# Optimization experiments

Hardware: AMD Instinct MI355X
Metric: run time of the kernel (lower is better)

## Reference

```python
import jax, jax.numpy as jnp
import numpy as np

N_NODES = 100000
N_EDGES = 1600000
D = 64
EPS_NORM = 1e-9
EPS_DENOM = 1e-9


def setup_inputs() -> dict:
    key = jax.random.key(0)
    k1, k2, k3, k4, k5 = jax.random.split(key, 5)
    x = jax.random.normal(k1, (N_NODES, D), dtype=jnp.float32)
    z = jax.random.normal(k2, (N_NODES, D), dtype=jnp.float32)
    edge_index = jax.random.randint(k3, (2, N_EDGES), 0, N_NODES, dtype=jnp.int64)
    W = jax.random.normal(k4, (D, D), dtype=jnp.float32) * (1.0 / np.sqrt(D))
    b = jax.random.normal(k5, (D,), dtype=jnp.float32) * 0.01
    alpha = jnp.ones((), dtype=jnp.float32)
    bias_edge = jnp.zeros((), dtype=jnp.float32)
    return {"x": x, "edge_index": edge_index, "z": z, "W": W, "b": b,
            "alpha": alpha, "bias_edge": bias_edge}


def reference(x, edge_index, z, W, b, alpha, bias_edge):
    row, col = edge_index[0], edge_index[1]
    z_i = z[row]                      # [E, D] gather
    z_j = z[col]                      # [E, D] gather
    num = jnp.sum(z_i * z_j, axis=-1)                       # [E]
    den = jnp.maximum(jnp.linalg.norm(z_i, axis=-1) * jnp.linalg.norm(z_j, axis=-1), EPS_NORM)
    corr = num / den                                        # cosine correlation per edge
    logits = alpha * corr + bias_edge                       # [E]
    exp_logits = jnp.exp(logits - jnp.max(logits))          # global-max-stabilized exp
    denom = jax.ops.segment_sum(exp_logits, row, num_segments=N_NODES)  # [N]
    attn = exp_logits / (denom[row] + EPS_DENOM)            # edge softmax over incoming edges
    msgs = attn[:, None] * x[col]                           # [E, D]
    out = jax.ops.segment_sum(msgs, row, num_segments=N_NODES)          # [N, D]
    return out @ W.T + b                                    # Linear(in_dim, out_dim)
```

## Files before the change

### kernel.cpp

```cpp
#include <hip/hip_runtime.h>
#include <hip/hip_fp16.h>
#include <math.h>

#define NN 100000
#define NE 1600000
#define D  64
#define NBLK 391

typedef _Float16 half2v __attribute__((ext_vector_type(2)));

__device__ __forceinline__ unsigned int pack_entry(int col, float ex) {
    unsigned short hb = __half_as_ushort(__float2half(ex));
    return ((unsigned int)col << 15) | (unsigned int)(hb & 0x7FFFu);
}
__device__ __forceinline__ float unpack_ex(unsigned int pk) {
    return __half2float(__ushort_as_half((unsigned short)(pk & 0x7FFFu)));
}

__global__ __launch_bounds__(256) void k_prep_count(const float* __restrict__ z,
                                                    const float* __restrict__ x,
                                                    const float* __restrict__ W,
                                                    __half* __restrict__ zx,
                                                    const int* __restrict__ ei,
                                                    int* __restrict__ cnt,
                                                    unsigned int* __restrict__ rankr) {
    __shared__ float Wt[64 * 65];
    for (int i = threadIdx.x; i < 4096; i += 256) {
        Wt[(i & 63) * 65 + (i >> 6)] = W[i];
    }
    __syncthreads();
    const int lane = threadIdx.x & 63;
    int wave = blockIdx.x * 4 + (threadIdx.x >> 6);
    int nWaves = gridDim.x * 4;
    for (int n = wave; n < NN; n += nWaves) {
        float zv = z[n * D + lane];
        float s = zv * zv;
#pragma unroll
        for (int off = 32; off; off >>= 1) s += __shfl_xor(s, off);
        float inv = 1.0f / sqrtf(fmaxf(s, 1e-18f));
        zx[(size_t)n * 128 + lane] = __float2half(zv * inv);
        float xv = x[n * D + lane];
        float y0 = 0.0f, y1 = 0.0f, y2 = 0.0f, y3 = 0.0f;
#pragma unroll
        for (int d = 0; d < 64; d += 4) {
            y0 = fmaf(__shfl(xv, d), Wt[d * 65 + lane], y0);
            y1 = fmaf(__shfl(xv, d + 1), Wt[(d + 1) * 65 + lane], y1);
            y2 = fmaf(__shfl(xv, d + 2), Wt[(d + 2) * 65 + lane], y2);
            y3 = fmaf(__shfl(xv, d + 3), Wt[(d + 3) * 65 + lane], y3);
        }
        zx[(size_t)n * 128 + 64 + lane] = __float2half((y0 + y1) + (y2 + y3));
    }
    int i = blockIdx.x * 256 + threadIdx.x;
    int stride = gridDim.x * 256;
    for (int e = i; e < NE; e += stride) {
        int r = __builtin_nontemporal_load(&ei[e]);
        int rk = atomicAdd(&cnt[r], 1);
        __builtin_nontemporal_store(((unsigned int)r << 15) | (unsigned int)rk, &rankr[e]);
    }
}

__global__ __launch_bounds__(256) void k_scan1(const int* __restrict__ cnt,
                                               int* __restrict__ inc,
                                               int* __restrict__ bsum) {
    __shared__ int sh[256];
    int gid = blockIdx.x * 256 + threadIdx.x;
    int v = (gid < NN) ? cnt[gid] : 0;
    sh[threadIdx.x] = v;
    __syncthreads();
    for (int off = 1; off < 256; off <<= 1) {
        int t = (threadIdx.x >= off) ? sh[threadIdx.x - off] : 0;
        __syncthreads();
        sh[threadIdx.x] += t;
        __syncthreads();
    }
    if (gid < NN) inc[gid] = sh[threadIdx.x];
    if (threadIdx.x == 255) bsum[blockIdx.x] = sh[255];
}

__global__ __launch_bounds__(512) void k_scan2(int* __restrict__ bsum) {
    __shared__ int sh[512];
    int v = (threadIdx.x < NBLK) ? bsum[threadIdx.x] : 0;
    sh[threadIdx.x] = v;
    __syncthreads();
    for (int off = 1; off < 512; off <<= 1) {
        int t = (threadIdx.x >= off) ? sh[threadIdx.x - off] : 0;
        __syncthreads();
        sh[threadIdx.x] += t;
        __syncthreads();
    }
    if (threadIdx.x < NBLK) bsum[threadIdx.x] = sh[threadIdx.x] - v;
}

__global__ __launch_bounds__(256) void k_scan3(const int* __restrict__ cnt,
                                               const int* __restrict__ inc,
                                               const int* __restrict__ bsum,
                                               int* __restrict__ row_start) {
    int gid = blockIdx.x * 256 + threadIdx.x;
    if (gid < NN) {
        row_start[gid] = inc[gid] - cnt[gid] + bsum[blockIdx.x];
    }
}

__global__ __launch_bounds__(256) void k_place(const int* __restrict__ ei,
                                               const unsigned int* __restrict__ rankr,
                                               const int* __restrict__ row_start,
                                               int* __restrict__ colidx) {
    int e = blockIdx.x * 256 + threadIdx.x;
    if (e >= NE) return;
    unsigned int rr = __builtin_nontemporal_load(&rankr[e]);
    int c = __builtin_nontemporal_load(&ei[NE + e]);
    int r = (int)(rr >> 15);
    int rk = (int)(rr & 0x7FFFu);
    __builtin_nontemporal_store(c, &colidx[row_start[r] + rk]);
}

__global__ __launch_bounds__(256) void k_node(const __half* __restrict__ zx,
                                              const int* __restrict__ colidx,
                                              const int* __restrict__ row_start,
                                              const int* __restrict__ cnt,
                                              const float* __restrict__ b,
                                              const float* __restrict__ alpha_p,
                                              const float* __restrict__ bias_p,
                                              float* __restrict__ out) {
    const int lane = threadIdx.x & 63;
    int n = (blockIdx.x * blockDim.x + threadIdx.x) >> 6;
    if (n >= NN) return;
    const float alpha = *alpha_p;
    const float bias = *bias_p;
    const float Mest = fabsf(alpha) + bias;
    int rs = row_start[n];
    int c = cnt[n];
    float bv = b[lane];
    const float4* zi4 = (const float4*)(zx + (size_t)n * 128);
    float4 zi[8];
#pragma unroll
    for (int k = 0; k < 8; ++k) zi[k] = zi4[k];
    float acc = 0.0f;
    float dsum = 0.0f;
    for (int base = 0; base < c; base += 64) {
        int m = min(64, c - base);
        int idx = base + lane;
        int col = (idx < c) ? colidx[rs + idx] : 0;
        const float4* zj4 = (const float4*)(zx + (size_t)col * 128);
        float4 zj[8];
#pragma unroll
        for (int k = 0; k < 8; ++k) zj[k] = zj4[k];
        float dot = 0.0f;
#pragma unroll
        for (int k = 0; k < 8; ++k) {
            const half2v* ha = (const half2v*)&zi[k];
            const half2v* hb = (const half2v*)&zj[k];
#pragma unroll
            for (int q = 0; q < 4; ++q) {
#if defined(__has_builtin) && __has_builtin(__builtin_amdgcn_fdot2)
                dot = __builtin_amdgcn_fdot2(ha[q], hb[q], dot, false);
#else
                float2 fa = __half22float2(*(const __half2*)&ha[q]);
                float2 fb = __half22float2(*(const __half2*)&hb[q]);
                dot = fmaf(fa.x, fb.x, dot);
                dot = fmaf(fa.y, fb.y, dot);
#endif
            }
        }
        float ex = (idx < c) ? __expf(alpha * dot + bias - Mest) : 0.0f;
        unsigned int pk = pack_entry(col, ex);
        float t = ex;
#pragma unroll
        for (int off = 32; off; off >>= 1) t += __shfl_xor(t, off);
        dsum += t;
        int j = 0;
        for (; j + 8 <= m; j += 8) {
            unsigned int p0 = (unsigned int)__builtin_amdgcn_readlane((int)pk, j);
            unsigned int p1 = (unsigned int)__builtin_amdgcn_readlane((int)pk, j + 1);
            unsigned int p2 = (unsigned int)__builtin_amdgcn_readlane((int)pk, j + 2);
            unsigned int p3 = (unsigned int)__builtin_amdgcn_readlane((int)pk, j + 3);
            unsigned int p4 = (unsigned int)__builtin_amdgcn_readlane((int)pk, j + 4);
            unsigned int p5 = (unsigned int)__builtin_amdgcn_readlane((int)pk, j + 5);
            unsigned int p6 = (unsigned int)__builtin_amdgcn_readlane((int)pk, j + 6);
            unsigned int p7 = (unsigned int)__builtin_amdgcn_readlane((int)pk, j + 7);
            float x0 = __half2float(zx[(size_t)(p0 >> 15) * 128 + 64 + lane]);
            float x1 = __half2float(zx[(size_t)(p1 >> 15) * 128 + 64 + lane]);
            float x2 = __half2float(zx[(size_t)(p2 >> 15) * 128 + 64 + lane]);
            float x3 = __half2float(zx[(size_t)(p3 >> 15) * 128 + 64 + lane]);
            float x4 = __half2float(zx[(size_t)(p4 >> 15) * 128 + 64 + lane]);
            float x5 = __half2float(zx[(size_t)(p5 >> 15) * 128 + 64 + lane]);
            float x6 = __half2float(zx[(size_t)(p6 >> 15) * 128 + 64 + lane]);
            float x7 = __half2float(zx[(size_t)(p7 >> 15) * 128 + 64 + lane]);
            acc = fmaf(unpack_ex(p0), x0, acc);
            acc = fmaf(unpack_ex(p1), x1, acc);
            acc = fmaf(unpack_ex(p2), x2, acc);
            acc = fmaf(unpack_ex(p3), x3, acc);
            acc = fmaf(unpack_ex(p4), x4, acc);
            acc = fmaf(unpack_ex(p5), x5, acc);
            acc = fmaf(unpack_ex(p6), x6, acc);
            acc = fmaf(unpack_ex(p7), x7, acc);
        }
        for (; j < m; ++j) {
            unsigned int p0 = (unsigned int)__builtin_amdgcn_readlane((int)pk, j);
            float x0 = __half2float(zx[(size_t)(p0 >> 15) * 128 + 64 + lane]);
            acc = fmaf(unpack_ex(p0), x0, acc);
        }
    }
    out[n * D + lane] = acc / (dsum + 1e-9f) + bv;
}

extern "C" void kernel_launch(void* const* d_in, const int* in_sizes, int n_in,
                              void* d_out, int out_size, void* d_ws, size_t ws_size,
                              hipStream_t stream) {
    const float* x = (const float*)d_in[0];
    const int* ei = (const int*)d_in[1];
    const float* z = (const float*)d_in[2];
    const float* W = (const float*)d_in[3];
    const float* b = (const float*)d_in[4];
    const float* alpha = (const float*)d_in[5];
    const float* bias_edge = (const float*)d_in[6];
    float* out = (float*)d_out;

    char* ws = (char*)d_ws;
    size_t off = 0;
    __half* zx = (__half*)(ws + off); off += (size_t)NN * 128 * 2;
    int* colidx = (int*)(ws + off); off += (size_t)NE * 4;
    unsigned int* rankr = (unsigned int*)(ws + off); off += (size_t)NE * 4;
    int* cnt = (int*)(ws + off); off += (size_t)NN * 4;
    int* inc = (int*)(ws + off); off += (size_t)NN * 4;
    int* row_start = (int*)(ws + off); off += (size_t)NN * 4;
    int* bsum = (int*)(ws + off); off += 512 * 4;

    hipMemsetAsync(cnt, 0, (size_t)NN * 4, stream);
    k_prep_count<<<4096, 256, 0, stream>>>(z, x, W, zx, ei, cnt, rankr);
    k_scan1<<<NBLK, 256, 0, stream>>>(cnt, inc, bsum);
    k_scan2<<<1, 512, 0, stream>>>(bsum);
    k_scan3<<<NBLK, 256, 0, stream>>>(cnt, inc, bsum, row_start);
    k_place<<<(NE + 255) / 256, 256, 0, stream>>>(ei, rankr, row_start, colidx);
    k_node<<<(NN * 64 + 255) / 256, 256, 0, stream>>>(zx, colidx, row_start, cnt, b, alpha, bias_edge, out);
}
```

Before: 260.8 us.

## Privatize per-row edge counters by XCD and use fp16 dot2 for x·W projection

After: 244.4 us. -6.3%, faster.

```diff
diff --git a/kernel.cpp b/kernel.cpp
--- a/kernel.cpp
+++ b/kernel.cpp
@@ -15,6 +15,17 @@
 }
 __device__ __forceinline__ float unpack_ex(unsigned int pk) {
     return __half2float(__ushort_as_half((unsigned short)(pk & 0x7FFFu)));
+}
+
+__device__ __forceinline__ float dot2acc(int a, unsigned int b, float c) {
+#if defined(__has_builtin) && __has_builtin(__builtin_amdgcn_fdot2)
+    return __builtin_amdgcn_fdot2(__builtin_bit_cast(half2v, a),
+                                  __builtin_bit_cast(half2v, b), c, false);
+#else
+    float2 fa = __half22float2(*(const __half2*)&a);
+    float2 fb = __half22float2(*(const __half2*)&b);
+    return fmaf(fa.y, fb.y, fmaf(fa.x, fb.x, c));
+#endif
 }
 
 __global__ __launch_bounds__(256) void k_prep_count(const float* __restrict__ z,
@@ -22,11 +33,19 @@
                                                     const float* __restrict__ W,
                                                     __half* __restrict__ zx,
                                                     const int* __restrict__ ei,
-                                                    int* __restrict__ cnt,
+                                                    int* __restrict__ cnt8,
                                                     unsigned int* __restrict__ rankr) {
-    __shared__ float Wt[64 * 65];
-    for (int i = threadIdx.x; i < 4096; i += 256) {
-        Wt[(i & 63) * 65 + (i >> 6)] = W[i];
+    __shared__ unsigned int WtP[32 * 64];
+    {
+        const float2* W2 = (const float2*)W;
+        for (int i = threadIdx.x; i < 2048; i += 256) {
+            int j = i >> 5, d2 = i & 31;
+            float2 wp = W2[j * 32 + d2];
+            half2v h;
+            h.x = (_Float16)wp.x;
+            h.y = (_Float16)wp.y;
+            WtP[d2 * 64 + j] = __builtin_bit_cast(unsigned int, h);
+        }
     }
     __syncthreads();
     const int lane = threadIdx.x & 63;
@@ -40,31 +59,43 @@
         float inv = 1.0f / sqrtf(fmaxf(s, 1e-18f));
         zx[(size_t)n * 128 + lane] = __float2half(zv * inv);
         float xv = x[n * D + lane];
-        float y0 = 0.0f, y1 = 0.0f, y2 = 0.0f, y3 = 0.0f;
-#pragma unroll
-        for (int d = 0; d < 64; d += 4) {
-            y0 = fmaf(__shfl(xv, d), Wt[d * 65 + lane], y0);
-            y1 = fmaf(__shfl(xv, d + 1), Wt[(d + 1) * 65 + lane], y1);
-            y2 = fmaf(__shfl(xv, d + 2), Wt[(d + 2) * 65 + lane], y2);
-            y3 = fmaf(__shfl(xv, d + 3), Wt[(d + 3) * 65 + lane], y3);
-        }
-        zx[(size_t)n * 128 + 64 + lane] = __float2half((y0 + y1) + (y2 + y3));
-    }
+        float pa = __shfl(xv, 2 * (lane & 31));
+        float pb = __shfl(xv, 2 * (lane & 31) + 1);
+        half2v pkh;
+        pkh.x = (_Float16)pa;
+        pkh.y = (_Float16)pb;
+        int pki = __builtin_bit_cast(int, pkh);
+        float y = 0.0f;
+#pragma unroll
+        for (int d2 = 0; d2 < 32; ++d2) {
+            int pv = __shfl(pki, d2);
+            unsigned int wv = WtP[d2 * 64 + lane];
+            y = dot2acc(pv, wv, y);
+        }
+        zx[(size_t)n * 128 + 64 + lane] = __float2half(y);
+    }
+    const int myc = (blockIdx.x & 7) * NN;
+    const unsigned int xcdbits = (unsigned int)(blockIdx.x & 7) << 12;
     int i = blockIdx.x * 256 + threadIdx.x;
     int stride = gridDim.x * 256;
     for (int e = i; e < NE; e += stride) {
         int r = __builtin_nontemporal_load(&ei[e]);
-        int rk = atomicAdd(&cnt[r], 1);
-        __builtin_nontemporal_store(((unsigned int)r << 15) | (unsigned int)rk, &rankr[e]);
-    }
-}
-
-__global__ __launch_bounds__(256) void k_scan1(const int* __restrict__ cnt,
+        int rk = atomicAdd(&cnt8[myc + r], 1);
+        __builtin_nontemporal_store(((unsigned int)r << 15) | xcdbits | (unsigned int)rk,
+                                    &rankr[e]);
+    }
+}
+
+__global__ __launch_bounds__(256) void k_scan1(const int* __restrict__ cnt8,
                                                int* __restrict__ inc,
                                                int* __restrict__ bsum) {
     __shared__ int sh[256];
     int gid = blockIdx.x * 256 + threadIdx.x;
-    int v = (gid < NN) ? cnt[gid] : 0;
+    int v = 0;
+    if (gid < NN) {
+#pragma unroll
+        for (int k = 0; k < 8; ++k) v += cnt8[k * NN + gid];
+    }
     sh[threadIdx.x] = v;
     __syncthreads();
     for (int off = 1; off < 256; off <<= 1) {
@@ -91,33 +122,50 @@
     if (threadIdx.x < NBLK) bsum[threadIdx.x] = sh[threadIdx.x] - v;
 }
 
-__global__ __launch_bounds__(256) void k_scan3(const int* __restrict__ cnt,
+__global__ __launch_bounds__(256) void k_scan3(const int* __restrict__ cnt8,
                                                const int* __restrict__ inc,
                                                const int* __restrict__ bsum,
-                                               int* __restrict__ row_start) {
+                                               int* __restrict__ row_start,
+                                               int* __restrict__ row_start8,
+                                               int* __restrict__ tot) {
     int gid = blockIdx.x * 256 + threadIdx.x;
-    if (gid < NN) {
-        row_start[gid] = inc[gid] - cnt[gid] + bsum[blockIdx.x];
+    if (gid >= NN) return;
+    int c[8];
+    int s8 = 0;
+#pragma unroll
+    for (int k = 0; k < 8; ++k) {
+        c[k] = cnt8[k * NN + gid];
+        s8 += c[k];
+    }
+    int ex = inc[gid] - s8 + bsum[blockIdx.x];
+    row_start[gid] = ex;
+    tot[gid] = s8;
+    int base = ex;
+#pragma unroll
+    for (int k = 0; k < 8; ++k) {
+        row_start8[k * NN + gid] = base;
+        base += c[k];
     }
 }
 
 __global__ __launch_bounds__(256) void k_place(const int* __restrict__ ei,
                                                const unsigned int* __restrict__ rankr,
-                                               const int* __restrict__ row_start,
+                                               const int* __restrict__ row_start8,
                                                int* __restrict__ colidx) {
     int e = blockIdx.x * 256 + threadIdx.x;
     if (e >= NE) return;
     unsigned int rr = __builtin_nontemporal_load(&rankr[e]);
     int c = __builtin_nontemporal_load(&ei[NE + e]);
     int r = (int)(rr >> 15);
-    int rk = (int)(rr & 0x7FFFu);
-    __builtin_nontemporal_store(c, &colidx[row_start[r] + rk]);
+    int xcd = (int)((rr >> 12) & 7u);
+    int rk = (int)(rr & 0xFFFu);
+    __builtin_nontemporal_store(c, &colidx[row_start8[xcd * NN + r] + rk]);
 }
 
 __global__ __launch_bounds__(256) void k_node(const __half* __restrict__ zx,
                                               const int* __restrict__ colidx,
                                               const int* __restrict__ row_start,
-                                              const int* __restrict__ cnt,
+                                              const int* __restrict__ tot,
                                               const float* __restrict__ b,
                                               const float* __restrict__ alpha_p,
                                               const float* __restrict__ bias_p,
@@ -129,7 +177,7 @@
     const float bias = *bias_p;
     const float Mest = fabsf(alpha) + bias;
     int rs = row_start[n];
-    int c = cnt[n];
+    int c = tot[n];
     float bv = b[lane];
     const float4* zi4 = (const float4*)(zx + (size_t)n * 128);
     float4 zi[8];
@@ -148,19 +196,10 @@
         float dot = 0.0f;
 #pragma unroll
         for (int k = 0; k < 8; ++k) {
-            const half2v* ha = (const half2v*)&zi[k];
-            const half2v* hb = (const half2v*)&zj[k];
-#pragma unroll
-            for (int q = 0; q < 4; ++q) {
-#if defined(__has_builtin) && __has_builtin(__builtin_amdgcn_fdot2)
-                dot = __builtin_amdgcn_fdot2(ha[q], hb[q], dot, false);
-#else
-                float2 fa = __half22float2(*(const __half2*)&ha[q]);
-                float2 fb = __half22float2(*(const __half2*)&hb[q]);
-                dot = fmaf(fa.x, fb.x, dot);
-                dot = fmaf(fa.y, fb.y, dot);
-#endif
-            }
+            const int* ha = (const int*)&zi[k];
+            const unsigned int* hb = (const unsigned int*)&zj[k];
+#pragma unroll
+            for (int q = 0; q < 4; ++q) dot = dot2acc(ha[q], hb[q], dot);
         }
         float ex = (idx < c) ? __expf(alpha * dot + bias - Mest) : 0.0f;
         unsigned int pk = pack_entry(col, ex);
@@ -221,16 +260,18 @@
     __half* zx = (__half*)(ws + off); off += (size_t)NN * 128 * 2;
     int* colidx = (int*)(ws + off); off += (size_t)NE * 4;
     unsigned int* rankr = (unsigned int*)(ws + off); off += (size_t)NE * 4;
-    int* cnt = (int*)(ws + off); off += (size_t)NN * 4;
+    int* cnt8 = (int*)(ws + off); off += (size_t)8 * NN * 4;
+    int* row_start8 = (int*)(ws + off); off += (size_t)8 * NN * 4;
     int* inc = (int*)(ws + off); off += (size_t)NN * 4;
     int* row_start = (int*)(ws + off); off += (size_t)NN * 4;
+    int* tot = (int*)(ws + off); off += (size_t)NN * 4;
     int* bsum = (int*)(ws + off); off += 512 * 4;
 
-    hipMemsetAsync(cnt, 0, (size_t)NN * 4, stream);
-    k_prep_count<<<4096, 256, 0, stream>>>(z, x, W, zx, ei, cnt, rankr);
-    k_scan1<<<NBLK, 256, 0, stream>>>(cnt, inc, bsum);
+    hipMemsetAsync(cnt8, 0, (size_t)8 * NN * 4, stream);
+    k_prep_count<<<4096, 256, 0, stream>>>(z, x, W, zx, ei, cnt8, rankr);
+    k_scan1<<<NBLK, 256, 0, stream>>>(cnt8, inc, bsum);
     k_scan2<<<1, 512, 0, stream>>>(bsum);
-    k_scan3<<<NBLK, 256, 0, stream>>>(cnt, inc, bsum, row_start);
-    k_place<<<(NE + 255) / 256, 256, 0, stream>>>(ei, rankr, row_start, colidx);
-    k_node<<<(NN * 64 + 255) / 256, 256, 0, stream>>>(zx, colidx, row_start, cnt, b, alpha, bias_edge, out);
-}
+    k_scan3<<<NBLK, 256, 0, stream>>>(cnt8, inc, bsum, row_start, row_start8, tot);
+    k_place<<<(NE + 255) / 256, 256, 0, stream>>>(ei, rankr, row_start8, colidx);
+    k_node<<<(NN * 64 + 255) / 256, 256, 0, stream>>>(zx, colidx, row_start, tot, b, alpha, bias_edge, out);
+}
```
